# Performance work log

Hardware: AMD Instinct MI355X
Metric: run time of the kernel (lower is better)

## Reference

```python
import jax, jax.numpy as jnp
import numpy as np

DIM = 1024
HEADS = 16
DIM_HEAD = 64
CHUNK = 64
INNER = HEADS * DIM_HEAD  # 1024


def setup_inputs() -> dict:
    key = jax.random.key(0)
    k1, k2, k3 = jax.random.split(key, 3)
    x = jax.random.normal(k1, (4, 4096, DIM), dtype=jnp.float32)
    # nn.Linear weights stored as (out, in); apply as x @ W.T
    w_qkv = jax.random.normal(k2, (INNER * 3, DIM), dtype=jnp.float32) * (DIM ** -0.5)
    w_out = jax.random.normal(k3, (DIM, INNER), dtype=jnp.float32) * (INNER ** -0.5)
    b_out = jnp.zeros((DIM,), dtype=jnp.float32)
    return {"x": x, "w_qkv": w_qkv, "w_out": w_out, "b_out": b_out}


def reference(x, w_qkv, w_out, b_out):
    b, n, _ = x.shape
    scale = DIM_HEAD ** -0.5
    qkv = jnp.einsum('bnd,ed->bne', x, w_qkv)  # (b, n, 3*inner)
    q, k, v = jnp.split(qkv, 3, axis=-1)
    nblk = n // CHUNK

    def to_blocks(t):
        # (b, n, h*d) -> (b, h, nblk, c, d)
        t = t.reshape(b, n, HEADS, DIM_HEAD).transpose(0, 2, 1, 3)
        return t.reshape(b, HEADS, nblk, CHUNK, DIM_HEAD)

    qb, kb, vb = to_blocks(q), to_blocks(k), to_blocks(v)
    scores = jnp.einsum('bhgqd,bhgkd->bhgqk', qb, kb) * scale  # block-local
    attn = jax.nn.softmax(scores, axis=-1)
    ob = jnp.einsum('bhgqk,bhgkd->bhgqd', attn, vb)
    out = ob.reshape(b, HEADS, n, DIM_HEAD).transpose(0, 2, 1, 3).reshape(b, n, INNER)
    return jnp.einsum('bne,de->bnd', out, w_out) + b_out
```

## Files before the change

### kernel.cpp

```cpp
#include <hip/hip_runtime.h>
#include <stdint.h>

typedef __attribute__((ext_vector_type(8))) short bf16x8;
typedef __attribute__((ext_vector_type(4))) float f32x4;

__device__ __forceinline__ unsigned short bf16_of(float f) {
  union { float f; uint32_t u; } x; x.f = f;
  uint32_t r = x.u + 0x7fffu + ((x.u >> 16) & 1u);
  return (unsigned short)(r >> 16);
}

#define GLD16(gp, lp) __builtin_amdgcn_global_load_lds( \
    (const __attribute__((address_space(1))) uint32_t*)(gp), \
    (__attribute__((address_space(3))) uint32_t*)(lp), 16, 0, 0)

__global__ void cvt_f32_bf16(const float* __restrict__ src,
                             unsigned short* __restrict__ dst, int n4) {
  int i = blockIdx.x * blockDim.x + threadIdx.x;
  int stride = gridDim.x * blockDim.x;
  for (int j = i; j < n4; j += stride) {
    float4 f = ((const float4*)src)[j];
    union { unsigned short s[4]; uint2 v; } u;
    u.s[0] = bf16_of(f.x); u.s[1] = bf16_of(f.y);
    u.s[2] = bf16_of(f.z); u.s[3] = bf16_of(f.w);
    ((uint2*)dst)[j] = u.v;
  }
}

template<int BIAS, int OUTF32>
__global__ __launch_bounds__(256, 2)
void gemm_bt(const unsigned short* __restrict__ A,
             const unsigned short* __restrict__ B,
             void* __restrict__ C, const float* __restrict__ bias,
             int N, int K)
{
  __shared__ __align__(1024) unsigned short As[128 * 64];
  __shared__ __align__(1024) unsigned short Bs[128 * 64];
  const int tid = threadIdx.x;
  const int w = tid >> 6, lane = tid & 63;
  const int bm0 = blockIdx.y * 128, bn0 = blockIdx.x * 128;
  const int wm = (w >> 1) * 64, wn = (w & 1) * 64;
  const int srow = lane >> 3;
  const int sc8 = lane & 7;

  f32x4 acc[4][4] = {};

  for (int k0 = 0; k0 < K; k0 += 64) {
    #pragma unroll
    for (int i = 0; i < 4; ++i) {
      const int chunk = i * 4 + w;
      const int row = chunk * 8 + srow;
      const int c8 = sc8 ^ (row & 7);
      GLD16(A + (size_t)(bm0 + row) * K + k0 + c8 * 8, (char*)As + chunk * 1024);
      GLD16(B + (size_t)(bn0 + row) * K + k0 + c8 * 8, (char*)Bs + chunk * 1024);
    }
    __syncthreads();
    {
      const int fr = lane & 15, kg = lane >> 4;
      #pragma unroll
      for (int kt = 0; kt < 2; ++kt) {
        bf16x8 av[4], bv[4];
        const int kb = kt * 64 + kg * 16;
        #pragma unroll
        for (int m = 0; m < 4; ++m) {
          const int r = wm + m * 16 + fr;
          av[m] = *(const bf16x8*)((const char*)As + r * 128 + (kb ^ ((r & 7) << 4)));
        }
        #pragma unroll
        for (int n = 0; n < 4; ++n) {
          const int r = wn + n * 16 + fr;
          bv[n] = *(const bf16x8*)((const char*)Bs + r * 128 + (kb ^ ((r & 7) << 4)));
        }
        #pragma unroll
        for (int m = 0; m < 4; ++m)
          #pragma unroll
          for (int n = 0; n < 4; ++n)
            acc[m][n] = __builtin_amdgcn_mfma_f32_16x16x32_bf16(av[m], bv[n], acc[m][n], 0, 0, 0);
      }
    }
    __syncthreads();
  }

  const int fr = lane & 15, rg = lane >> 4;
  #pragma unroll
  for (int m = 0; m < 4; ++m) {
    #pragma unroll
    for (int n = 0; n < 4; ++n) {
      #pragma unroll
      for (int r = 0; r < 4; ++r) {
        const int row = bm0 + wm + m * 16 + rg * 4 + r;
        const int col = bn0 + wn + n * 16 + fr;
        float v = acc[m][n][r];
        if (OUTF32) {
          float bb = BIAS ? bias[col] : 0.0f;
          ((float*)C)[(size_t)row * N + col] = v + bb;
        } else {
          ((unsigned short*)C)[(size_t)row * N + col] = bf16_of(v);
        }
      }
    }
  }
}

__global__ __launch_bounds__(256, 2)
void attn_block(const unsigned short* __restrict__ qkv,
                unsigned short* __restrict__ o)
{
  __shared__ __align__(1024) unsigned short Qs[64 * 64];
  __shared__ __align__(1024) unsigned short Ks[64 * 64];
  __shared__ __align__(1024) unsigned short Vt[64 * 64];
  __shared__ __align__(1024) unsigned short Ps[64 * 64];
  const int tid = threadIdx.x, w = tid >> 6, lane = tid & 63;
  const int g = blockIdx.x, h = blockIdx.y, b = blockIdx.z;
  const size_t mbase = (size_t)b * 4096 + (size_t)g * 64;
  const unsigned short* qg = qkv + mbase * 3072 + h * 64;
  const unsigned short* kgl = qkv + mbase * 3072 + 1024 + h * 64;
  const unsigned short* vg = qkv + mbase * 3072 + 2048 + h * 64;

  #pragma unroll
  for (int i = 0; i < 2; ++i) {
    const int chunk = i * 4 + w;
    const int row = chunk * 8 + (lane >> 3);
    const int c8 = (lane & 7) ^ (row & 7);
    GLD16(qg + (size_t)row * 3072 + c8 * 8, (char*)Qs + chunk * 1024);
    GLD16(kgl + (size_t)row * 3072 + c8 * 8, (char*)Ks + chunk * 1024);
  }
  #pragma unroll
  for (int i = 0; i < 2; ++i) {
    const int c = i * 256 + tid;
    const int n = c >> 3, d0 = (c & 7) * 8;
    bf16x8 v = *(const bf16x8*)(vg + (size_t)n * 3072 + d0);
    #pragma unroll
    for (int j = 0; j < 8; ++j) {
      const int d = d0 + j;
      const int bo = d * 128 + n * 2;
      *(unsigned short*)((char*)Vt + (bo ^ ((d & 7) << 4))) = (unsigned short)v[j];
    }
  }
  __syncthreads();

  const int fr = lane & 15, kg = lane >> 4;
  f32x4 s[4] = {};
  #pragma unroll
  for (int kt = 0; kt < 2; ++kt) {
    const int kb = kt * 64 + kg * 16;
    const int rq = w * 16 + fr;
    bf16x8 aq = *(const bf16x8*)((const char*)Qs + rq * 128 + (kb ^ ((rq & 7) << 4)));
    #pragma unroll
    for (int nf = 0; nf < 4; ++nf) {
      const int rk = nf * 16 + fr;
      bf16x8 bk = *(const bf16x8*)((const char*)Ks + rk * 128 + (kb ^ ((rk & 7) << 4)));
      s[nf] = __builtin_amdgcn_mfma_f32_16x16x32_bf16(aq, bk, s[nf], 0, 0, 0);
    }
  }

  const float scale = 0.125f;
  float inv[4];
  #pragma unroll
  for (int r = 0; r < 4; ++r) {
    float m0 = fmaxf(fmaxf(s[0][r], s[1][r]), fmaxf(s[2][r], s[3][r]));
    #pragma unroll
    for (int d = 1; d < 16; d <<= 1) m0 = fmaxf(m0, __shfl_xor(m0, d));
    float sum = 0.0f;
    #pragma unroll
    for (int nf = 0; nf < 4; ++nf) {
      float p = __expf((s[nf][r] - m0) * scale);
      s[nf][r] = p;
      sum += p;
    }
    #pragma unroll
    for (int d = 1; d < 16; d <<= 1) sum += __shfl_xor(sum, d);
    inv[r] = 1.0f / sum;
  }

  #pragma unroll
  for (int r = 0; r < 4; ++r) {
    const int m = w * 16 + kg * 4 + r;
    #pragma unroll
    for (int nf = 0; nf < 4; ++nf) {
      const int bo = m * 128 + (nf * 16 + fr) * 2;
      *(unsigned short*)((char*)Ps + (bo ^ ((m & 7) << 4))) = bf16_of(s[nf][r] * inv[r]);
    }
  }
  __syncthreads();

  f32x4 oa[4] = {};
  #pragma unroll
  for (int kt = 0; kt < 2; ++kt) {
    const int kb = kt * 64 + kg * 16;
    const int rp = w * 16 + fr;
    bf16x8 ap = *(const bf16x8*)((const char*)Ps + rp * 128 + (kb ^ ((rp & 7) << 4)));
    #pragma unroll
    for (int df = 0; df < 4; ++df) {
      const int rv = df * 16 + fr;
      bf16x8 bv = *(const bf16x8*)((const char*)Vt + rv * 128 + (kb ^ ((rv & 7) << 4)));
      oa[df] = __builtin_amdgcn_mfma_f32_16x16x32_bf16(ap, bv, oa[df], 0, 0, 0);
    }
  }
  #pragma unroll
  for (int df = 0; df < 4; ++df) {
    #pragma unroll
    for (int r = 0; r < 4; ++r) {
      const size_t row = mbase + w * 16 + kg * 4 + r;
      const int col = h * 64 + df * 16 + fr;
      o[row * 1024 + col] = bf16_of(oa[df][r]);
    }
  }
}

extern "C" void kernel_launch(void* const* d_in, const int* in_sizes, int n_in,
                              void* d_out, int out_size, void* d_ws, size_t ws_size,
                              hipStream_t stream) {
  const float* x     = (const float*)d_in[0];
  const float* w_qkv = (const float*)d_in[1];
  const float* w_out = (const float*)d_in[2];
  const float* b_out = (const float*)d_in[3];
  char* ws = (char*)d_ws;
  const size_t SZ_X  = (size_t)16384 * 1024 * 2;
  const size_t SZ_WQ = (size_t)3072 * 1024 * 2;
  const size_t SZ_WO = (size_t)1024 * 1024 * 2;
  unsigned short* xb  = (unsigned short*)ws;
  unsigned short* wqb = (unsigned short*)(ws + SZ_X);
  unsigned short* wob = (unsigned short*)(ws + SZ_X + SZ_WQ);
  unsigned short* qkv = (unsigned short*)(ws + SZ_X + SZ_WQ + SZ_WO);
  unsigned short* ob  = xb;

  cvt_f32_bf16<<<2048, 256, 0, stream>>>(x, xb, 16384 * 1024 / 4);
  cvt_f32_bf16<<<512, 256, 0, stream>>>(w_qkv, wqb, 3072 * 1024 / 4);
  cvt_f32_bf16<<<256, 256, 0, stream>>>(w_out, wob, 1024 * 1024 / 4);
  gemm_bt<0,0><<<dim3(24, 128), 256, 0, stream>>>(xb, wqb, qkv, nullptr, 3072, 1024);
  attn_block<<<dim3(64, 16, 4), 256, 0, stream>>>(qkv, ob);
  gemm_bt<1,1><<<dim3(8, 128), 256, 0, stream>>>(ob, wob, d_out, b_out, 1024, 1024);
}
```

Baseline: 203.0 us.

## Replace GEMM with 256x256 tile, double-buffered, 8-wave pipelined kernel

Replaces the 128x128 single-buffered GEMM with a 256x256 tile kernel using 512 threads and 128KB of LDS double buffering. Global-to-LDS loads for the next K-steps are issued in quarter-tile pieces between the MFMA phases, paced with explicit vmcnt waits and barriers. MFMA sections are wrapped in setprio, and block IDs are remapped to group tiles for cache locality. The goal is to hide load latency and raise arithmetic intensity, at the cost of heavy LDS use (one block per CU) and fragile hand-tuned synchronisation.

```diff
diff --git a/kernel.cpp b/kernel.cpp
--- a/kernel.cpp
+++ b/kernel.cpp
@@ -13,6 +13,8 @@
 #define GLD16(gp, lp) __builtin_amdgcn_global_load_lds( \
     (const __attribute__((address_space(1))) uint32_t*)(gp), \
     (__attribute__((address_space(3))) uint32_t*)(lp), 16, 0, 0)
+
+#define BAR() do { asm volatile("" ::: "memory"); __builtin_amdgcn_s_barrier(); asm volatile("" ::: "memory"); } while (0)
 
 __global__ void cvt_f32_bf16(const float* __restrict__ src,
                              unsigned short* __restrict__ dst, int n4) {
@@ -28,75 +30,149 @@
 }
 
 template<int BIAS, int OUTF32>
-__global__ __launch_bounds__(256, 2)
-void gemm_bt(const unsigned short* __restrict__ A,
+__global__ __launch_bounds__(512, 2)
+void gemm256(const unsigned short* __restrict__ A,
              const unsigned short* __restrict__ B,
              void* __restrict__ C, const float* __restrict__ bias,
-             int N, int K)
+             int M, int N, int K)
 {
-  __shared__ __align__(1024) unsigned short As[128 * 64];
-  __shared__ __align__(1024) unsigned short Bs[128 * 64];
-  const int tid = threadIdx.x;
-  const int w = tid >> 6, lane = tid & 63;
-  const int bm0 = blockIdx.y * 128, bn0 = blockIdx.x * 128;
-  const int wm = (w >> 1) * 64, wn = (w & 1) * 64;
-  const int srow = lane >> 3;
-  const int sc8 = lane & 7;
-
-  f32x4 acc[4][4] = {};
-
-  for (int k0 = 0; k0 < K; k0 += 64) {
-    #pragma unroll
-    for (int i = 0; i < 4; ++i) {
-      const int chunk = i * 4 + w;
-      const int row = chunk * 8 + srow;
-      const int c8 = sc8 ^ (row & 7);
-      GLD16(A + (size_t)(bm0 + row) * K + k0 + c8 * 8, (char*)As + chunk * 1024);
-      GLD16(B + (size_t)(bn0 + row) * K + k0 + c8 * 8, (char*)Bs + chunk * 1024);
-    }
-    __syncthreads();
-    {
-      const int fr = lane & 15, kg = lane >> 4;
-      #pragma unroll
-      for (int kt = 0; kt < 2; ++kt) {
-        bf16x8 av[4], bv[4];
-        const int kb = kt * 64 + kg * 16;
-        #pragma unroll
-        for (int m = 0; m < 4; ++m) {
-          const int r = wm + m * 16 + fr;
-          av[m] = *(const bf16x8*)((const char*)As + r * 128 + (kb ^ ((r & 7) << 4)));
-        }
-        #pragma unroll
-        for (int n = 0; n < 4; ++n) {
-          const int r = wn + n * 16 + fr;
-          bv[n] = *(const bf16x8*)((const char*)Bs + r * 128 + (kb ^ ((r & 7) << 4)));
-        }
-        #pragma unroll
-        for (int m = 0; m < 4; ++m)
-          #pragma unroll
-          for (int n = 0; n < 4; ++n)
-            acc[m][n] = __builtin_amdgcn_mfma_f32_16x16x32_bf16(av[m], bv[n], acc[m][n], 0, 0, 0);
-      }
-    }
-    __syncthreads();
-  }
-
-  const int fr = lane & 15, rg = lane >> 4;
-  #pragma unroll
-  for (int m = 0; m < 4; ++m) {
-    #pragma unroll
-    for (int n = 0; n < 4; ++n) {
-      #pragma unroll
-      for (int r = 0; r < 4; ++r) {
-        const int row = bm0 + wm + m * 16 + rg * 4 + r;
-        const int col = bn0 + wn + n * 16 + fr;
-        float v = acc[m][n][r];
-        if (OUTF32) {
-          float bb = BIAS ? bias[col] : 0.0f;
-          ((float*)C)[(size_t)row * N + col] = v + bb;
-        } else {
-          ((unsigned short*)C)[(size_t)row * N + col] = bf16_of(v);
-        }
+  __shared__ __align__(1024) unsigned short sm[65536];
+  char* const smb = (char*)sm;
+  const int tid = threadIdx.x, w = tid >> 6, lane = tid & 63;
+  const int wm = w >> 2, wn = w & 3;
+  const int fr = lane & 15, kg = lane >> 4;
+  const int swz = (fr & 7) << 4;
+  const int srow = lane >> 3, sslot = lane & 7;
+
+  const int nbx = N >> 8;
+  const int nwg = gridDim.x;
+  const int bid = blockIdx.x;
+  const int bid2 = (bid & 7) * (nwg >> 3) + (bid >> 3);
+  const int bm0 = (bid2 / nbx) << 8;
+  const int bn0 = (bid2 % nbx) << 8;
+  const int NT = K >> 6;
+
+  f32x4 acc[8][4] = {};
+
+  auto STAGE = [&](int buf, int opnd, int half, int kt) {
+    const unsigned short* G = opnd ? B : A;
+    const int grow0 = opnd ? bn0 : bm0;
+    char* region = smb + opnd * 65536 + buf * 32768 + half * 16384;
+    const int k0 = kt << 6;
+    #pragma unroll
+    for (int i = 0; i < 2; ++i) {
+      const int c = i * 8 + w;
+      const int row = half * 128 + c * 8 + srow;
+      const int slot = sslot ^ srow;
+      GLD16(G + (size_t)(grow0 + row) * K + k0 + slot * 8, region + c * 1024);
+    }
+  };
+  auto LDA = [&](char* Ab, int j, int ks) -> bf16x8 {
+    const int r = 32 * j + 16 * wm + fr;
+    return *(const bf16x8*)(Ab + r * 128 + ((ks * 64 + kg * 16) ^ swz));
+  };
+  auto LDB = [&](char* Bb, int l, int ks) -> bf16x8 {
+    const int r = 64 * l + 16 * wn + fr;
+    return *(const bf16x8*)(Bb + r * 128 + ((ks * 64 + kg * 16) ^ swz));
+  };
+
+  STAGE(0, 0, 0, 0);
+  STAGE(0, 1, 1, 0);
+  STAGE(0, 0, 1, 0);
+  STAGE(0, 1, 0, 0);
+  if (NT > 1) {
+    STAGE(1, 0, 0, 1);
+    STAGE(1, 1, 1, 1);
+    asm volatile("s_waitcnt vmcnt(4)" ::: "memory");
+  } else {
+    asm volatile("s_waitcnt vmcnt(0)" ::: "memory");
+  }
+  BAR();
+
+  for (int t = 0; t < NT; ++t) {
+    char* Ab = smb + (t & 1) * 32768;
+    char* Bb = smb + 65536 + (t & 1) * 32768;
+    bf16x8 a[4][2], b[2][2];
+
+    #pragma unroll
+    for (int j = 0; j < 4; ++j) { a[j][0] = LDA(Ab, j, 0); a[j][1] = LDA(Ab, j, 1); }
+    #pragma unroll
+    for (int l = 0; l < 2; ++l) { b[l][0] = LDB(Bb, l, 0); b[l][1] = LDB(Bb, l, 1); }
+    if (t + 1 < NT) STAGE((t + 1) & 1, 0, 1, t + 1);
+    BAR();
+    __builtin_amdgcn_s_setprio(1);
+    #pragma unroll
+    for (int j = 0; j < 4; ++j)
+      #pragma unroll
+      for (int l = 0; l < 2; ++l) {
+        acc[j][l] = __builtin_amdgcn_mfma_f32_16x16x32_bf16(a[j][0], b[l][0], acc[j][l], 0, 0, 0);
+        acc[j][l] = __builtin_amdgcn_mfma_f32_16x16x32_bf16(a[j][1], b[l][1], acc[j][l], 0, 0, 0);
+      }
+    __builtin_amdgcn_s_setprio(0);
+    BAR();
+
+    #pragma unroll
+    for (int l = 0; l < 2; ++l) { b[l][0] = LDB(Bb, l + 2, 0); b[l][1] = LDB(Bb, l + 2, 1); }
+    if (t + 1 < NT) STAGE((t + 1) & 1, 1, 0, t + 1);
+    BAR();
+    __builtin_amdgcn_s_setprio(1);
+    #pragma unroll
+    for (int j = 0; j < 4; ++j)
+      #pragma unroll
+      for (int l = 0; l < 2; ++l) {
+        acc[j][l + 2] = __builtin_amdgcn_mfma_f32_16x16x32_bf16(a[j][0], b[l][0], acc[j][l + 2], 0, 0, 0);
+        acc[j][l + 2] = __builtin_amdgcn_mfma_f32_16x16x32_bf16(a[j][1], b[l][1], acc[j][l + 2], 0, 0, 0);
+      }
+    __builtin_amdgcn_s_setprio(0);
+    BAR();
+
+    #pragma unroll
+    for (int j = 0; j < 4; ++j) { a[j][0] = LDA(Ab, j + 4, 0); a[j][1] = LDA(Ab, j + 4, 1); }
+    if (t + 2 < NT) STAGE(t & 1, 0, 0, t + 2);
+    BAR();
+    __builtin_amdgcn_s_setprio(1);
+    #pragma unroll
+    for (int j = 0; j < 4; ++j)
+      #pragma unroll
+      for (int l = 0; l < 2; ++l) {
+        acc[j + 4][l + 2] = __builtin_amdgcn_mfma_f32_16x16x32_bf16(a[j][0], b[l][0], acc[j + 4][l + 2], 0, 0, 0);
+        acc[j + 4][l + 2] = __builtin_amdgcn_mfma_f32_16x16x32_bf16(a[j][1], b[l][1], acc[j + 4][l + 2], 0, 0, 0);
+      }
+    __builtin_amdgcn_s_setprio(0);
+    BAR();
+
+    #pragma unroll
+    for (int l = 0; l < 2; ++l) { b[l][0] = LDB(Bb, l, 0); b[l][1] = LDB(Bb, l, 1); }
+    if (t + 2 < NT) STAGE(t & 1, 1, 1, t + 2);
+    BAR();
+    __builtin_amdgcn_s_setprio(1);
+    #pragma unroll
+    for (int j = 0; j < 4; ++j)
+      #pragma unroll
+      for (int l = 0; l < 2; ++l) {
+        acc[j + 4][l] = __builtin_amdgcn_mfma_f32_16x16x32_bf16(a[j][0], b[l][0], acc[j + 4][l], 0, 0, 0);
+        acc[j + 4][l] = __builtin_amdgcn_mfma_f32_16x16x32_bf16(a[j][1], b[l][1], acc[j + 4][l], 0, 0, 0);
+      }
+    __builtin_amdgcn_s_setprio(0);
+    if (t + 2 < NT) { asm volatile("s_waitcnt vmcnt(4)" ::: "memory"); }
+    else            { asm volatile("s_waitcnt vmcnt(0)" ::: "memory"); }
+    BAR();
+  }
+
+  #pragma unroll
+  for (int l = 0; l < 4; ++l) {
+    const int col = bn0 + 64 * l + 16 * wn + fr;
+    float bb = 0.0f;
+    if (BIAS && OUTF32) bb = bias[col];
+    #pragma unroll
+    for (int j = 0; j < 8; ++j) {
+      const int row0 = bm0 + 32 * j + 16 * wm + kg * 4;
+      #pragma unroll
+      for (int rr = 0; rr < 4; ++rr) {
+        if (OUTF32)
+          ((float*)C)[(size_t)(row0 + rr) * N + col] = acc[j][l][rr] + bb;
+        else
+          ((unsigned short*)C)[(size_t)(row0 + rr) * N + col] = bf16_of(acc[j][l][rr]);
       }
     }
   }
@@ -228,7 +304,7 @@
   cvt_f32_bf16<<<2048, 256, 0, stream>>>(x, xb, 16384 * 1024 / 4);
   cvt_f32_bf16<<<512, 256, 0, stream>>>(w_qkv, wqb, 3072 * 1024 / 4);
   cvt_f32_bf16<<<256, 256, 0, stream>>>(w_out, wob, 1024 * 1024 / 4);
-  gemm_bt<0,0><<<dim3(24, 128), 256, 0, stream>>>(xb, wqb, qkv, nullptr, 3072, 1024);
+  gemm256<0,0><<<dim3(768), 512, 0, stream>>>(xb, wqb, qkv, nullptr, 16384, 3072, 1024);
   attn_block<<<dim3(64, 16, 4), 256, 0, stream>>>(qkv, ob);
-  gemm_bt<1,1><<<dim3(8, 128), 256, 0, stream>>>(ob, wob, d_out, b_out, 1024, 1024);
-}
+  gemm256<1,1><<<dim3(256), 512, 0, stream>>>(ob, wob, d_out, b_out, 16384, 1024, 1024);
+}
```

Measured after the change: 212.8 us. 4.8% more time.

## Double-buffer GEMM LDS loads with XCD-aware tile mapping and coalesced attention stores

Applied to the files above, without the earlier changes.

The GEMM now double-buffers its A and B tiles in 64KB of LDS, issuing the next k-tile's global-to-LDS loads right after reading the current tile into registers. This uses one barrier per iteration instead of two and raises wave priority around the MFMA block. Tiles are remapped over a 1D grid so each XCD gets a contiguous group of N tiles for better L2 reuse. The attention kernel stages its bf16 output through a swizzled LDS tile so it can write 16-byte vector stores instead of scattered 2-byte stores. The larger LDS footprint may reduce occupancy.

```diff
diff --git a/kernel.cpp b/kernel.cpp
--- a/kernel.cpp
+++ b/kernel.cpp
@@ -13,6 +13,8 @@
 #define GLD16(gp, lp) __builtin_amdgcn_global_load_lds( \
     (const __attribute__((address_space(1))) uint32_t*)(gp), \
     (__attribute__((address_space(3))) uint32_t*)(lp), 16, 0, 0)
+
+#define BAR() do { asm volatile("" ::: "memory"); __builtin_amdgcn_s_barrier(); asm volatile("" ::: "memory"); } while (0)
 
 __global__ void cvt_f32_bf16(const float* __restrict__ src,
                              unsigned short* __restrict__ dst, int n4) {
@@ -27,76 +29,97 @@
   }
 }
 
-template<int BIAS, int OUTF32>
+template<int BIAS, int OUTF32, int GW>
 __global__ __launch_bounds__(256, 2)
-void gemm_bt(const unsigned short* __restrict__ A,
+void gemm128(const unsigned short* __restrict__ A,
              const unsigned short* __restrict__ B,
              void* __restrict__ C, const float* __restrict__ bias,
              int N, int K)
 {
-  __shared__ __align__(1024) unsigned short As[128 * 64];
-  __shared__ __align__(1024) unsigned short Bs[128 * 64];
-  const int tid = threadIdx.x;
-  const int w = tid >> 6, lane = tid & 63;
-  const int bm0 = blockIdx.y * 128, bn0 = blockIdx.x * 128;
-  const int wm = (w >> 1) * 64, wn = (w & 1) * 64;
-  const int srow = lane >> 3;
-  const int sc8 = lane & 7;
+  __shared__ __align__(1024) unsigned short sm[32768];
+  char* const smb = (char*)sm;
+  const int tid = threadIdx.x, w = tid >> 6, lane = tid & 63;
+  const int wm = w >> 1, wn = w & 1;
+  const int fr = lane & 15, kg = lane >> 4;
+  const int swz = (fr & 7) << 4;
+  const int srow = lane >> 3, sslot = lane & 7;
+  const int cXcd = blockIdx.x & 7, iIdx = blockIdx.x >> 3;
+  const int mt = iIdx / GW, nt = cXcd * GW + iIdx % GW;
+  const int NT = K >> 6;
+
+  int stOff[4];
+  #pragma unroll
+  for (int i = 0; i < 4; ++i)
+    stOff[i] = ((i * 4 + w) * 8 + srow) * K + (sslot ^ srow) * 8;
+
+  const unsigned short* aBase = A + ((size_t)mt << 7) * K;
+  const unsigned short* bBase = B + ((size_t)nt << 7) * K;
+
+  auto STAGE = [&](const unsigned short* src, int opnd, int parity) {
+    char* region = smb + opnd * 32768 + parity * 16384;
+    #pragma unroll
+    for (int i = 0; i < 4; ++i)
+      GLD16(src + stOff[i], region + (i * 4 + w) * 1024);
+  };
+  auto LDA = [&](char* Ab, int m, int kk) -> bf16x8 {
+    const int r = wm * 64 + m * 16 + fr;
+    return *(const bf16x8*)(Ab + r * 128 + ((kk * 64 + kg * 16) ^ ((r & 7) << 4)));
+  };
+  auto LDB = [&](char* Bb, int n, int kk) -> bf16x8 {
+    const int r = wn * 64 + n * 16 + fr;
+    return *(const bf16x8*)(Bb + r * 128 + ((kk * 64 + kg * 16) ^ ((r & 7) << 4)));
+  };
 
   f32x4 acc[4][4] = {};
 
-  for (int k0 = 0; k0 < K; k0 += 64) {
-    #pragma unroll
-    for (int i = 0; i < 4; ++i) {
-      const int chunk = i * 4 + w;
-      const int row = chunk * 8 + srow;
-      const int c8 = sc8 ^ (row & 7);
-      GLD16(A + (size_t)(bm0 + row) * K + k0 + c8 * 8, (char*)As + chunk * 1024);
-      GLD16(B + (size_t)(bn0 + row) * K + k0 + c8 * 8, (char*)Bs + chunk * 1024);
-    }
-    __syncthreads();
-    {
-      const int fr = lane & 15, kg = lane >> 4;
+  STAGE(bBase, 1, 0);
+  STAGE(aBase, 0, 0);
+
+  for (int t = 0; t < NT; ++t) {
+    char* Ab = smb + (t & 1) * 16384;
+    char* Bb = smb + 32768 + (t & 1) * 16384;
+
+    asm volatile("s_waitcnt vmcnt(0)" ::: "memory");
+    BAR();
+
+    bf16x8 a[4][2], bb[4][2];
+    #pragma unroll
+    for (int n = 0; n < 4; ++n) { bb[n][0] = LDB(Bb, n, 0); bb[n][1] = LDB(Bb, n, 1); }
+    #pragma unroll
+    for (int m = 0; m < 4; ++m) { a[m][0] = LDA(Ab, m, 0); a[m][1] = LDA(Ab, m, 1); }
+
+    if (t + 1 < NT) {
+      const int p1 = (t + 1) & 1;
+      STAGE(bBase + ((t + 1) << 6), 1, p1);
+      STAGE(aBase + ((t + 1) << 6), 0, p1);
+    }
+
+    __builtin_amdgcn_s_setprio(1);
+    #pragma unroll
+    for (int kk = 0; kk < 2; ++kk)
       #pragma unroll
-      for (int kt = 0; kt < 2; ++kt) {
-        bf16x8 av[4], bv[4];
-        const int kb = kt * 64 + kg * 16;
+      for (int m = 0; m < 4; ++m)
         #pragma unroll
-        for (int m = 0; m < 4; ++m) {
-          const int r = wm + m * 16 + fr;
-          av[m] = *(const bf16x8*)((const char*)As + r * 128 + (kb ^ ((r & 7) << 4)));
-        }
-        #pragma unroll
-        for (int n = 0; n < 4; ++n) {
-          const int r = wn + n * 16 + fr;
-          bv[n] = *(const bf16x8*)((const char*)Bs + r * 128 + (kb ^ ((r & 7) << 4)));
-        }
-        #pragma unroll
-        for (int m = 0; m < 4; ++m)
-          #pragma unroll
-          for (int n = 0; n < 4; ++n)
-            acc[m][n] = __builtin_amdgcn_mfma_f32_16x16x32_bf16(av[m], bv[n], acc[m][n], 0, 0, 0);
-      }
-    }
-    __syncthreads();
-  }
-
-  const int fr = lane & 15, rg = lane >> 4;
-  #pragma unroll
-  for (int m = 0; m < 4; ++m) {
-    #pragma unroll
-    for (int n = 0; n < 4; ++n) {
+        for (int n = 0; n < 4; ++n)
+          acc[m][n] = __builtin_amdgcn_mfma_f32_16x16x32_bf16(a[m][kk], bb[n][kk], acc[m][n], 0, 0, 0);
+    __builtin_amdgcn_s_setprio(0);
+  }
+
+  const int bm0 = mt << 7, bn0 = nt << 7;
+  #pragma unroll
+  for (int n = 0; n < 4; ++n) {
+    const int col = bn0 + wn * 64 + n * 16 + fr;
+    float bb2 = 0.0f;
+    if (BIAS && OUTF32) bb2 = bias[col];
+    #pragma unroll
+    for (int m = 0; m < 4; ++m) {
+      const int row0 = bm0 + wm * 64 + m * 16 + kg * 4;
       #pragma unroll
-      for (int r = 0; r < 4; ++r) {
-        const int row = bm0 + wm + m * 16 + rg * 4 + r;
-        const int col = bn0 + wn + n * 16 + fr;
-        float v = acc[m][n][r];
-        if (OUTF32) {
-          float bb = BIAS ? bias[col] : 0.0f;
-          ((float*)C)[(size_t)row * N + col] = v + bb;
-        } else {
-          ((unsigned short*)C)[(size_t)row * N + col] = bf16_of(v);
-        }
+      for (int rr = 0; rr < 4; ++rr) {
+        if (OUTF32)
+          ((float*)C)[(size_t)(row0 + rr) * N + col] = acc[m][n][rr] + bb2;
+        else
+          ((unsigned short*)C)[(size_t)(row0 + rr) * N + col] = bf16_of(acc[m][n][rr]);
       }
     }
   }
@@ -110,6 +133,7 @@
   __shared__ __align__(1024) unsigned short Ks[64 * 64];
   __shared__ __align__(1024) unsigned short Vt[64 * 64];
   __shared__ __align__(1024) unsigned short Ps[64 * 64];
+  __shared__ __align__(1024) unsigned short Os[64 * 64];
   const int tid = threadIdx.x, w = tid >> 6, lane = tid & 63;
   const int g = blockIdx.x, h = blockIdx.y, b = blockIdx.z;
   const size_t mbase = (size_t)b * 4096 + (size_t)g * 64;
@@ -197,14 +221,27 @@
       oa[df] = __builtin_amdgcn_mfma_f32_16x16x32_bf16(ap, bv, oa[df], 0, 0, 0);
     }
   }
+
   #pragma unroll
   for (int df = 0; df < 4; ++df) {
     #pragma unroll
     for (int r = 0; r < 4; ++r) {
-      const size_t row = mbase + w * 16 + kg * 4 + r;
-      const int col = h * 64 + df * 16 + fr;
-      o[row * 1024 + col] = bf16_of(oa[df][r]);
-    }
+      const int m = w * 16 + kg * 4 + r;
+      const int bo = m * 128 + (df * 16 + fr) * 2;
+      *(unsigned short*)((char*)Os + (bo ^ ((m & 7) << 4))) = bf16_of(oa[df][r]);
+    }
+  }
+  __syncthreads();
+  {
+    const int row = tid >> 2;
+    const int sb = (tid & 3) * 32;
+    const int sw = (row & 7) << 4;
+    char* rp = (char*)Os + row * 128;
+    uint4 v0 = *(uint4*)(rp + (sb ^ sw));
+    uint4 v1 = *(uint4*)(rp + ((sb + 16) ^ sw));
+    char* op = (char*)(o + (mbase + row) * 1024 + h * 64) + sb;
+    *(uint4*)op = v0;
+    *(uint4*)(op + 16) = v1;
   }
 }
 
@@ -228,7 +265,7 @@
   cvt_f32_bf16<<<2048, 256, 0, stream>>>(x, xb, 16384 * 1024 / 4);
   cvt_f32_bf16<<<512, 256, 0, stream>>>(w_qkv, wqb, 3072 * 1024 / 4);
   cvt_f32_bf16<<<256, 256, 0, stream>>>(w_out, wob, 1024 * 1024 / 4);
-  gemm_bt<0,0><<<dim3(24, 128), 256, 0, stream>>>(xb, wqb, qkv, nullptr, 3072, 1024);
+  gemm128<0,0,3><<<dim3(3072), 256, 0, stream>>>(xb, wqb, qkv, nullptr, 3072, 1024);
   attn_block<<<dim3(64, 16, 4), 256, 0, stream>>>(qkv, ob);
-  gemm_bt<1,1><<<dim3(8, 128), 256, 0, stream>>>(ob, wob, d_out, b_out, 1024, 1024);
-}
+  gemm128<1,1,1><<<dim3(1024), 256, 0, stream>>>(ob, wob, d_out, b_out, 1024, 1024);
+}
```

After: 207.0 us. Within noise of the previous version (+2.0%).
